# Kernel optimization log

Hardware: AMD Instinct MI355X
Metric: run time of the kernel (lower is better)

Reference implementation:

```python
import jax, jax.numpy as jnp
from jax import lax
import numpy as np

DIM = 384
HEADS = 8
B, H, W = 8, 128, 128
_DN = ('NCHW', 'OIHW', 'NCHW')


def setup_inputs() -> dict:
    key = jax.random.key(0)
    ks = jax.random.split(key, 8)
    x = jax.random.normal(ks[0], (B, DIM, H, W), jnp.float32)
    qkv_w = jax.random.normal(ks[1], (3 * DIM, DIM, 1, 1), jnp.float32) * 0.02
    qkv_b = jax.random.normal(ks[2], (3 * DIM,), jnp.float32) * 0.02
    dw_w = jax.random.normal(ks[3], (3 * DIM, 1, 3, 3), jnp.float32) * 0.02
    dw_b = jax.random.normal(ks[4], (3 * DIM,), jnp.float32) * 0.02
    proj_w = jax.random.normal(ks[5], (DIM, DIM, 1, 1), jnp.float32) * 0.02
    proj_b = jax.random.normal(ks[6], (DIM,), jnp.float32) * 0.02
    temperature = jnp.ones((HEADS, 1, 1), jnp.float32)
    return {"x": x, "qkv_w": qkv_w, "qkv_b": qkv_b, "dw_w": dw_w,
            "dw_b": dw_b, "proj_w": proj_w, "proj_b": proj_b,
            "temperature": temperature}


def _l2norm(t, eps=1e-12):
    # F.normalize(t, dim=-1): divide by max(||t||_2, eps)
    n = jnp.sqrt(jnp.sum(t * t, axis=-1, keepdims=True))
    return t / jnp.maximum(n, eps)


def reference(x, qkv_w, qkv_b, dw_w, dw_b, proj_w, proj_b, temperature):
    b, C, h, w = x.shape
    heads = HEADS
    c = C // heads
    hw = h * w
    # 1x1 pointwise qkv conv
    qkv = lax.conv_general_dilated(x, qkv_w, (1, 1), 'VALID',
                                   dimension_numbers=_DN) + qkv_b[None, :, None, None]
    # 3x3 depthwise conv, padding=1
    qkv = lax.conv_general_dilated(qkv, dw_w, (1, 1), ((1, 1), (1, 1)),
                                   feature_group_count=3 * C,
                                   dimension_numbers=_DN) + dw_b[None, :, None, None]
    q, k, v = jnp.split(qkv, 3, axis=1)
    # b (head c) h w -> b head c (h w)
    q = q.reshape(b, heads, c, hw)
    k = k.reshape(b, heads, c, hw)
    v = v.reshape(b, heads, c, hw)
    q = _l2norm(q)
    k = _l2norm(k)
    # processor scales q by temperature*sqrt(hw); SDPA divides by sqrt(hw):
    # net logits = temperature * q_n @ k_n^T  (CxC channel attention per head)
    temp = temperature.reshape(1, heads, 1, 1)
    logits = jnp.einsum('bhcn,bhdn->bhcd', q * temp, k)
    attn = jax.nn.softmax(logits, axis=-1)
    out = jnp.einsum('bhcd,bhdn->bhcn', attn, v)  # [b, heads, c, hw]
    out = out.reshape(b, C, h, w)
    return lax.conv_general_dilated(out, proj_w, (1, 1), 'VALID',
                                    dimension_numbers=_DN) + proj_b[None, :, None, None]
```

## Files before the change

kernel.cpp:

```cpp
#include <hip/hip_runtime.h>
#include <hip/hip_bf16.h>
#include <cstdint>


#define BATCH 8
#define DIM 384
#define HEADS 8
#define CH 48
#define HW 16384
#define C3 1152

typedef __attribute__((ext_vector_type(8))) short bf16x8;
typedef __attribute__((ext_vector_type(8))) unsigned short u16x8;
typedef __attribute__((ext_vector_type(4))) float f32x4;

__device__ __forceinline__ float b2f(ushort b) {
  union { float f; unsigned u; } x; x.u = ((unsigned)b) << 16; return x.f;
}
__device__ __forceinline__ ushort f2b(float f) {
  union { float f; unsigned u; } x; x.f = f;
  unsigned r = x.u + 0x7fffu + ((x.u >> 16) & 1u);
  return (ushort)(r >> 16);
}

__device__ __forceinline__ void async16(const ushort* g, ushort* l) {
  __builtin_amdgcn_global_load_lds(
      (const __attribute__((address_space(1))) unsigned int*)(unsigned long long)(uintptr_t)g,
      (__attribute__((address_space(3))) unsigned int*)(unsigned int)(uintptr_t)l,
      16, 0, 0);
}

__global__ __launch_bounds__(256) void cast_w(const float* __restrict__ s,
                                              ushort* __restrict__ d, int n) {
  int i = (blockIdx.x * 256 + threadIdx.x) * 4;
  if (i + 3 < n) {
    float4 v = *(const float4*)(s + i);
    ushort4 o = make_ushort4(f2b(v.x), f2b(v.y), f2b(v.z), f2b(v.w));
    *(ushort4*)(d + i) = o;
  }
}

template <typename SrcT, int OUT_BF16>
__global__ __launch_bounds__(512) void gemm_px(
    const ushort* __restrict__ A, const SrcT* __restrict__ src,
    const float* __restrict__ bias, void* __restrict__ Cout,
    int M, long Asb, long Ssb, long Csb) {
  constexpr int K = DIM;
  constexpr int BP = 392;
  int zb = blockIdx.y;
  int px0 = blockIdx.x * 128;
  const ushort* Ab = A + (size_t)zb * Asb;
  const SrcT* Sb = src + (size_t)zb * Ssb;
  __shared__ __align__(16) ushort Bs[128 * BP];
  __shared__ __align__(16) ushort As[2][128 * 64];
  int tid = threadIdx.x, lane = tid & 63, wid = tid >> 6;
  int wm = wid >> 1, wn = wid & 1;
  int fr = lane & 15, fs = lane >> 4;

  {
    int pix = tid & 127;
    int cg = tid >> 7;
#pragma unroll
    for (int rr = 0; rr < 12; ++rr) {
      int c8 = cg + rr * 4;
      u16x8 pk;
#pragma unroll
      for (int j = 0; j < 8; ++j) {
        int c = c8 * 8 + j;
        if constexpr (sizeof(SrcT) == 4)
          pk[j] = f2b(((const float*)Sb)[(size_t)c * HW + px0 + pix]);
        else
          pk[j] = ((const ushort*)Sb)[(size_t)c * HW + px0 + pix];
      }
      *(u16x8*)&Bs[pix * BP + c8 * 8] = pk;
    }
  }

  auto stageA = [&](int buf, int mt, int k0) {
#pragma unroll
    for (int q = 0; q < 2; ++q) {
      int r = q * 64 + wid * 8 + (lane >> 3);
      int col = ((lane & 7) ^ (r & 7)) * 8;
      async16(Ab + (size_t)(mt * 128 + r) * K + k0 + col,
              &As[buf][(q * 64 + wid * 8) * 64]);
    }
  };

  f32x4 acc[2][4];
  auto compute = [&](int buf, int k0) {
#pragma unroll
    for (int kk = 0; kk < 2; ++kk) {
      bf16x8 af[2], bv[4];
#pragma unroll
      for (int m = 0; m < 2; ++m) {
        int R = wm * 32 + m * 16 + fr;
        int slot = kk * 4 + fs;
        af[m] = *(const bf16x8*)&As[buf][R * 64 + ((slot ^ (R & 7)) << 3)];
      }
#pragma unroll
      for (int n = 0; n < 4; ++n) {
        int P = wn * 64 + n * 16 + fr;
        bv[n] = *(const bf16x8*)&Bs[P * BP + k0 + kk * 32 + (fs << 3)];
      }
#pragma unroll
      for (int m = 0; m < 2; ++m)
#pragma unroll
        for (int n = 0; n < 4; ++n)
          acc[m][n] = __builtin_amdgcn_mfma_f32_16x16x32_bf16(af[m], bv[n], acc[m][n], 0, 0, 0);
    }
  };

  const int MT = M >> 7;
  stageA(0, 0, 0);
  __syncthreads();

  for (int mt = 0; mt < MT; ++mt) {
    f32x4 zero = {0.f, 0.f, 0.f, 0.f};
#pragma unroll
    for (int m = 0; m < 2; ++m)
#pragma unroll
      for (int n = 0; n < 4; ++n) acc[m][n] = zero;
#pragma unroll
    for (int t = 0; t < 5; ++t) {
      stageA((t + 1) & 1, mt, (t + 1) * 64);
      __builtin_amdgcn_s_setprio(1);
      compute(t & 1, t * 64);
      __builtin_amdgcn_s_setprio(0);
      __syncthreads();
    }
    if (mt + 1 < MT) stageA(0, mt + 1, 0);
    __builtin_amdgcn_s_setprio(1);
    compute(1, 320);
    __builtin_amdgcn_s_setprio(0);
#pragma unroll
    for (int m = 0; m < 2; ++m)
#pragma unroll
      for (int j = 0; j < 4; ++j) {
        int gr = mt * 128 + wm * 32 + m * 16 + fs * 4 + j;
        float bz = bias[gr];
#pragma unroll
        for (int n = 0; n < 4; ++n) {
          int gc = px0 + wn * 64 + n * 16 + fr;
          float v = acc[m][n][j] + bz;
          if constexpr (OUT_BF16)
            ((ushort*)Cout)[(size_t)zb * Csb + (size_t)gr * HW + gc] = f2b(v);
          else
            ((float*)Cout)[(size_t)zb * Csb + (size_t)gr * HW + gc] = v;
        }
      }
    __syncthreads();
  }
}

__global__ __launch_bounds__(256) void dwconv(
    const ushort* __restrict__ in, const float* __restrict__ w9,
    const float* __restrict__ b9, ushort* __restrict__ out,
    float* __restrict__ sq) {
  int ch = blockIdx.x;
  int b = blockIdx.y;
  const size_t plane = ((size_t)b * C3 + ch) * HW;
  int tid = threadIdx.x, lane = tid & 63;
  int rg = tid >> 4, cg = tid & 15;
  int r0 = rg * 8, c0 = cg * 8;

  float w[9];
#pragma unroll
  for (int i = 0; i < 9; ++i) w[i] = w9[ch * 9 + i];
  float bias = b9[ch];

  float a0[8], a1[8];
#pragma unroll
  for (int c = 0; c < 8; ++c) { a0[c] = 0.f; a1[c] = 0.f; }
  float ss = 0.f;

#pragma unroll
  for (int it = 0; it < 10; ++it) {
    int r = r0 - 1 + it;
    float x[8];
    if ((unsigned)r < 128u) {
      u16x8 raw = *(const u16x8*)(in + plane + (size_t)r * 128 + c0);
#pragma unroll
      for (int c = 0; c < 8; ++c) x[c] = b2f(raw[c]);
    } else {
#pragma unroll
      for (int c = 0; c < 8; ++c) x[c] = 0.f;
    }
    float xl = __shfl(x[7], lane - 1);
    float xr = __shfl(x[0], lane + 1);
    if (cg == 0) xl = 0.f;
    if (cg == 15) xr = 0.f;

    float h0[8], h1[8], h2[8];
#pragma unroll
    for (int c = 0; c < 8; ++c) {
      float l = (c == 0) ? xl : x[c - 1];
      float rt = (c == 7) ? xr : x[c + 1];
      h0[c] = w[0] * l + w[1] * x[c] + w[2] * rt;
      h1[c] = w[3] * l + w[4] * x[c] + w[5] * rt;
      h2[c] = w[6] * l + w[7] * x[c] + w[8] * rt;
    }
    if (it >= 2) {
      int R = r - 1;
      u16x8 pk;
#pragma unroll
      for (int c = 0; c < 8; ++c) {
        float o = a0[c] + h2[c] + bias;
        ss += o * o;
        pk[c] = f2b(o);
      }
      *(u16x8*)(out + plane + (size_t)R * 128 + c0) = pk;
    }
#pragma unroll
    for (int c = 0; c < 8; ++c) { a0[c] = a1[c] + h1[c]; a1[c] = h0[c]; }
  }

  if (ch < 2 * DIM) {
#pragma unroll
    for (int off = 32; off; off >>= 1) ss += __shfl_down(ss, off, 64);
    if (lane == 0) atomicAdd(&sq[b * 2 * DIM + ch], ss);
  }
}

__global__ __launch_bounds__(256) void gram(const ushort* __restrict__ qkvd,
                                            float* __restrict__ G) {
  int chunk = blockIdx.x;
  int bh = blockIdx.y;
  int b = bh >> 3, h = bh & 7;
  int tid = threadIdx.x, lane = tid & 63, wid = tid >> 6;
  const ushort* qbase = qkvd + ((size_t)b * C3 + h * CH) * HW;
  const ushort* kbase = qbase + (size_t)DIM * HW;
  int pix0 = chunk * 1024 + wid * 256;
  int fr = lane & 15, fk = (lane >> 4) * 8;
  f32x4 zero = {0.f, 0.f, 0.f, 0.f};
  f32x4 acc[3][3];
#pragma unroll
  for (int i = 0; i < 3; ++i)
#pragma unroll
    for (int j = 0; j < 3; ++j) acc[i][j] = zero;
#pragma unroll
  for (int it = 0; it < 8; ++it) {
    int pix = pix0 + it * 32 + fk;
    bf16x8 aq[3], bk[3];
#pragma unroll
    for (int mi = 0; mi < 3; ++mi)
      aq[mi] = *(const bf16x8*)(qbase + (size_t)(mi * 16 + fr) * HW + pix);
#pragma unroll
    for (int ni = 0; ni < 3; ++ni)
      bk[ni] = *(const bf16x8*)(kbase + (size_t)(ni * 16 + fr) * HW + pix);
#pragma unroll
    for (int mi = 0; mi < 3; ++mi)
#pragma unroll
      for (int ni = 0; ni < 3; ++ni)
        acc[mi][ni] = __builtin_amdgcn_mfma_f32_16x16x32_bf16(aq[mi], bk[ni], acc[mi][ni], 0, 0, 0);
  }
  __shared__ float gs[CH * CH];
  for (int i = tid; i < CH * CH; i += 256) gs[i] = 0.f;
  __syncthreads();
  int crow = (lane >> 4) * 4, ccol = lane & 15;
#pragma unroll
  for (int mi = 0; mi < 3; ++mi)
#pragma unroll
    for (int ni = 0; ni < 3; ++ni)
#pragma unroll
      for (int j = 0; j < 4; ++j)
        atomicAdd(&gs[(mi * 16 + crow + j) * CH + ni * 16 + ccol], acc[mi][ni][j]);
  __syncthreads();
  float* Gp = G + (size_t)bh * CH * CH;
  for (int i = tid; i < CH * CH; i += 256) atomicAdd(&Gp[i], gs[i]);
}

__global__ void softmax_k(const float* __restrict__ G, const float* __restrict__ sq,
                          const float* __restrict__ temp, float* __restrict__ attn) {
  int bh = blockIdx.x, b = bh >> 3, h = bh & 7;
  int lane = threadIdx.x;
  __shared__ float inq[CH], ink[CH];
  if (lane < CH) {
    inq[lane] = 1.f / fmaxf(sqrtf(sq[b * 2 * DIM + h * CH + lane]), 1e-12f);
    ink[lane] = 1.f / fmaxf(sqrtf(sq[b * 2 * DIM + DIM + h * CH + lane]), 1e-12f);
  }
  __syncthreads();
  if (lane < CH) {
    float t = temp[h] * inq[lane];
    const float* g = G + (size_t)bh * CH * CH + lane * CH;
    float v[CH];
    float mx = -1e30f;
#pragma unroll
    for (int d = 0; d < CH; ++d) { v[d] = t * g[d] * ink[d]; mx = fmaxf(mx, v[d]); }
    float s = 0.f;
#pragma unroll
    for (int d = 0; d < CH; ++d) { v[d] = expf(v[d] - mx); s += v[d]; }
    float inv = 1.f / s;
    float* a = attn + (size_t)bh * CH * CH + lane * CH;
#pragma unroll
    for (int d = 0; d < CH; ++d) a[d] = v[d] * inv;
  }
}

__global__ __launch_bounds__(384) void weff_k(const float* __restrict__ pw,
                                              const float* __restrict__ attn,
                                              ushort* __restrict__ weff) {
  int dg = threadIdx.x;
  int p = blockIdx.x;
  int b = blockIdx.y;
  int h = dg / CH, d = dg - h * CH;
  const float* a = attn + (((size_t)b * HEADS + h) * CH) * CH + d;
  const float* wrow = pw + (size_t)p * DIM + h * CH;
  float s = 0.f;
#pragma unroll
  for (int c = 0; c < CH; ++c) s += wrow[c] * a[c * CH];
  weff[((size_t)b * DIM + p) * DIM + dg] = f2b(s);
}

extern "C" void kernel_launch(void* const* d_in, const int* in_sizes, int n_in,
                              void* d_out, int out_size, void* d_ws, size_t ws_size,
                              hipStream_t stream) {
  const float* x = (const float*)d_in[0];
  const float* qkv_w = (const float*)d_in[1];
  const float* qkv_b = (const float*)d_in[2];
  const float* dw_w = (const float*)d_in[3];
  const float* dw_b = (const float*)d_in[4];
  const float* proj_w = (const float*)d_in[5];
  const float* proj_b = (const float*)d_in[6];
  const float* temp = (const float*)d_in[7];

  const size_t SZ_C1 = (size_t)BATCH * C3 * HW * 2;
  const size_t SZ_WQB = (size_t)C3 * DIM * 2;
  const size_t SZ_SQ = (size_t)BATCH * 2 * DIM * 4;
  const size_t SZ_G = (size_t)BATCH * HEADS * CH * CH * 4;

  const size_t OFF_C1 = 0;
  const size_t OFF_QKVD = OFF_C1 + SZ_C1;
  const size_t OFF_WQB = OFF_QKVD + SZ_C1;
  const size_t OFF_SQ = OFF_WQB + SZ_WQB;
  const size_t OFF_G = OFF_SQ + SZ_SQ;
  const size_t OFF_ATTN = OFF_G + SZ_G;
  const size_t OFF_WEFF = OFF_ATTN + SZ_G;
  const size_t TOTAL = OFF_WEFF + (size_t)BATCH * DIM * DIM * 2;
  if (ws_size < TOTAL) return;

  char* ws = (char*)d_ws;
  ushort* c1 = (ushort*)(ws + OFF_C1);
  ushort* qkvd = (ushort*)(ws + OFF_QKVD);
  ushort* wqb = (ushort*)(ws + OFF_WQB);
  float* sq = (float*)(ws + OFF_SQ);
  float* G = (float*)(ws + OFF_G);
  float* attn = (float*)(ws + OFF_ATTN);
  ushort* weff = (ushort*)(ws + OFF_WEFF);

  hipMemsetAsync(ws + OFF_SQ, 0, SZ_SQ + SZ_G, stream);

  cast_w<<<(C3 * DIM) / 1024, 256, 0, stream>>>(qkv_w, wqb, C3 * DIM);
  gemm_px<float, 1><<<dim3(HW / 128, BATCH), 512, 0, stream>>>(
      wqb, x, qkv_b, (void*)c1, C3, 0L, (long)DIM * HW, (long)C3 * HW);
  dwconv<<<dim3(C3, BATCH), 256, 0, stream>>>(c1, dw_w, dw_b, qkvd, sq);
  gram<<<dim3(16, BATCH * HEADS), 256, 0, stream>>>(qkvd, G);
  softmax_k<<<BATCH * HEADS, 64, 0, stream>>>(G, sq, temp, attn);
  weff_k<<<dim3(DIM, BATCH), 384, 0, stream>>>(proj_w, attn, weff);
  gemm_px<ushort, 0><<<dim3(HW / 128, BATCH), 512, 0, stream>>>(
      weff, qkvd + (size_t)2 * DIM * HW, proj_b, d_out, DIM,
      (long)DIM * DIM, (long)C3 * HW, (long)DIM * HW);
}
```

Before: 543.5 us.

## Enlarge GEMM M-tile to 256 with padded weights and XOR-swizzled B tile

Each block of the pointwise GEMMs now computes 256 output rows per M-step instead of 128, doubling the accumulator tile per wave to raise MFMA work per B-fragment load. The padded B tile (stride 392) is replaced by an unpadded 384-stride layout with an XOR swizzle to avoid LDS bank conflicts while saving shared memory. M is padded (1280 for qkv, 512 for proj) and stores are masked by the real row count, which wastes MFMA work on the padded rows (notably for the proj GEMM, 512 vs 384). The padded weight rows are never written, so they hold uninitialized workspace data, but their outputs are masked off. Shared memory grows and launch bounds force one block per CU.

```diff
diff --git a/kernel.cpp b/kernel.cpp
--- a/kernel.cpp
+++ b/kernel.cpp
@@ -9,6 +9,8 @@
 #define CH 48
 #define HW 16384
 #define C3 1152
+#define MPAD1 1280
+#define WPAD 512
 
 typedef __attribute__((ext_vector_type(8))) short bf16x8;
 typedef __attribute__((ext_vector_type(8))) unsigned short u16x8;
@@ -41,18 +43,17 @@
 }
 
 template <typename SrcT, int OUT_BF16>
-__global__ __launch_bounds__(512) void gemm_px(
+__global__ __launch_bounds__(512, 1) void gemm_px2(
     const ushort* __restrict__ A, const SrcT* __restrict__ src,
     const float* __restrict__ bias, void* __restrict__ Cout,
-    int M, long Asb, long Ssb, long Csb) {
+    int Mpad, int Mreal, long Asb, long Ssb, long Csb) {
   constexpr int K = DIM;
-  constexpr int BP = 392;
   int zb = blockIdx.y;
   int px0 = blockIdx.x * 128;
   const ushort* Ab = A + (size_t)zb * Asb;
   const SrcT* Sb = src + (size_t)zb * Ssb;
-  __shared__ __align__(16) ushort Bs[128 * BP];
-  __shared__ __align__(16) ushort As[2][128 * 64];
+  __shared__ __align__(16) ushort Bs[128 * 384];
+  __shared__ __align__(16) ushort As[2][256 * 64];
   int tid = threadIdx.x, lane = tid & 63, wid = tid >> 6;
   int wm = wid >> 1, wn = wid & 1;
   int fr = lane & 15, fs = lane >> 4;
@@ -72,80 +73,83 @@
         else
           pk[j] = ((const ushort*)Sb)[(size_t)c * HW + px0 + pix];
       }
-      *(u16x8*)&Bs[pix * BP + c8 * 8] = pk;
+      *(u16x8*)&Bs[pix * 384 + ((c8 ^ (pix & 7)) << 3)] = pk;
     }
   }
 
   auto stageA = [&](int buf, int mt, int k0) {
 #pragma unroll
-    for (int q = 0; q < 2; ++q) {
+    for (int q = 0; q < 4; ++q) {
       int r = q * 64 + wid * 8 + (lane >> 3);
       int col = ((lane & 7) ^ (r & 7)) * 8;
-      async16(Ab + (size_t)(mt * 128 + r) * K + k0 + col,
+      async16(Ab + (size_t)(mt * 256 + r) * K + k0 + col,
               &As[buf][(q * 64 + wid * 8) * 64]);
     }
   };
 
-  f32x4 acc[2][4];
-  auto compute = [&](int buf, int k0) {
+  f32x4 acc[4][4];
+  auto compute = [&](int buf, int t) {
 #pragma unroll
     for (int kk = 0; kk < 2; ++kk) {
-      bf16x8 af[2], bv[4];
-#pragma unroll
-      for (int m = 0; m < 2; ++m) {
-        int R = wm * 32 + m * 16 + fr;
+      bf16x8 af[4], bv[4];
+#pragma unroll
+      for (int m = 0; m < 4; ++m) {
+        int R = wm * 64 + m * 16 + fr;
         int slot = kk * 4 + fs;
         af[m] = *(const bf16x8*)&As[buf][R * 64 + ((slot ^ (R & 7)) << 3)];
       }
 #pragma unroll
       for (int n = 0; n < 4; ++n) {
         int P = wn * 64 + n * 16 + fr;
-        bv[n] = *(const bf16x8*)&Bs[P * BP + k0 + kk * 32 + (fs << 3)];
-      }
-#pragma unroll
-      for (int m = 0; m < 2; ++m)
+        int gslot = t * 8 + kk * 4 + fs;
+        bv[n] = *(const bf16x8*)&Bs[P * 384 + ((gslot ^ (P & 7)) << 3)];
+      }
+#pragma unroll
+      for (int m = 0; m < 4; ++m)
 #pragma unroll
         for (int n = 0; n < 4; ++n)
           acc[m][n] = __builtin_amdgcn_mfma_f32_16x16x32_bf16(af[m], bv[n], acc[m][n], 0, 0, 0);
     }
   };
 
-  const int MT = M >> 7;
+  const int MT = Mpad >> 8;
   stageA(0, 0, 0);
   __syncthreads();
 
   for (int mt = 0; mt < MT; ++mt) {
     f32x4 zero = {0.f, 0.f, 0.f, 0.f};
 #pragma unroll
-    for (int m = 0; m < 2; ++m)
+    for (int m = 0; m < 4; ++m)
 #pragma unroll
       for (int n = 0; n < 4; ++n) acc[m][n] = zero;
 #pragma unroll
     for (int t = 0; t < 5; ++t) {
       stageA((t + 1) & 1, mt, (t + 1) * 64);
       __builtin_amdgcn_s_setprio(1);
-      compute(t & 1, t * 64);
+      compute(t & 1, t);
       __builtin_amdgcn_s_setprio(0);
       __syncthreads();
     }
     if (mt + 1 < MT) stageA(0, mt + 1, 0);
     __builtin_amdgcn_s_setprio(1);
-    compute(1, 320);
+    compute(1, 5);
     __builtin_amdgcn_s_setprio(0);
 #pragma unroll
-    for (int m = 0; m < 2; ++m)
+    for (int m = 0; m < 4; ++m)
 #pragma unroll
       for (int j = 0; j < 4; ++j) {
-        int gr = mt * 128 + wm * 32 + m * 16 + fs * 4 + j;
-        float bz = bias[gr];
-#pragma unroll
-        for (int n = 0; n < 4; ++n) {
-          int gc = px0 + wn * 64 + n * 16 + fr;
-          float v = acc[m][n][j] + bz;
-          if constexpr (OUT_BF16)
-            ((ushort*)Cout)[(size_t)zb * Csb + (size_t)gr * HW + gc] = f2b(v);
-          else
-            ((float*)Cout)[(size_t)zb * Csb + (size_t)gr * HW + gc] = v;
+        int gr = mt * 256 + wm * 64 + m * 16 + fs * 4 + j;
+        if (gr < Mreal) {
+          float bz = bias[gr];
+#pragma unroll
+          for (int n = 0; n < 4; ++n) {
+            int gc = px0 + wn * 64 + n * 16 + fr;
+            float v = acc[m][n][j] + bz;
+            if constexpr (OUT_BF16)
+              ((ushort*)Cout)[(size_t)zb * Csb + (size_t)gr * HW + gc] = f2b(v);
+            else
+              ((float*)Cout)[(size_t)zb * Csb + (size_t)gr * HW + gc] = v;
+          }
         }
       }
     __syncthreads();
@@ -308,7 +312,7 @@
   float s = 0.f;
 #pragma unroll
   for (int c = 0; c < CH; ++c) s += wrow[c] * a[c * CH];
-  weff[((size_t)b * DIM + p) * DIM + dg] = f2b(s);
+  weff[((size_t)b * WPAD + p) * DIM + dg] = f2b(s);
 }
 
 extern "C" void kernel_launch(void* const* d_in, const int* in_sizes, int n_in,
@@ -324,9 +328,10 @@
   const float* temp = (const float*)d_in[7];
 
   const size_t SZ_C1 = (size_t)BATCH * C3 * HW * 2;
-  const size_t SZ_WQB = (size_t)C3 * DIM * 2;
+  const size_t SZ_WQB = (size_t)MPAD1 * DIM * 2;
   const size_t SZ_SQ = (size_t)BATCH * 2 * DIM * 4;
   const size_t SZ_G = (size_t)BATCH * HEADS * CH * CH * 4;
+  const size_t SZ_WEFF = (size_t)BATCH * WPAD * DIM * 2;
 
   const size_t OFF_C1 = 0;
   const size_t OFF_QKVD = OFF_C1 + SZ_C1;
@@ -335,7 +340,7 @@
   const size_t OFF_G = OFF_SQ + SZ_SQ;
   const size_t OFF_ATTN = OFF_G + SZ_G;
   const size_t OFF_WEFF = OFF_ATTN + SZ_G;
-  const size_t TOTAL = OFF_WEFF + (size_t)BATCH * DIM * DIM * 2;
+  const size_t TOTAL = OFF_WEFF + SZ_WEFF;
   if (ws_size < TOTAL) return;
 
   char* ws = (char*)d_ws;
@@ -350,13 +355,13 @@
   hipMemsetAsync(ws + OFF_SQ, 0, SZ_SQ + SZ_G, stream);
 
   cast_w<<<(C3 * DIM) / 1024, 256, 0, stream>>>(qkv_w, wqb, C3 * DIM);
-  gemm_px<float, 1><<<dim3(HW / 128, BATCH), 512, 0, stream>>>(
-      wqb, x, qkv_b, (void*)c1, C3, 0L, (long)DIM * HW, (long)C3 * HW);
+  gemm_px2<float, 1><<<dim3(HW / 128, BATCH), 512, 0, stream>>>(
+      wqb, x, qkv_b, (void*)c1, MPAD1, C3, 0L, (long)DIM * HW, (long)C3 * HW);
   dwconv<<<dim3(C3, BATCH), 256, 0, stream>>>(c1, dw_w, dw_b, qkvd, sq);
   gram<<<dim3(16, BATCH * HEADS), 256, 0, stream>>>(qkvd, G);
   softmax_k<<<BATCH * HEADS, 64, 0, stream>>>(G, sq, temp, attn);
   weff_k<<<dim3(DIM, BATCH), 384, 0, stream>>>(proj_w, attn, weff);
-  gemm_px<ushort, 0><<<dim3(HW / 128, BATCH), 512, 0, stream>>>(
-      weff, qkvd + (size_t)2 * DIM * HW, proj_b, d_out, DIM,
-      (long)DIM * DIM, (long)C3 * HW, (long)DIM * HW);
-}
+  gemm_px2<ushort, 0><<<dim3(HW / 128, BATCH), 512, 0, stream>>>(
+      weff, qkvd + (size_t)2 * DIM * HW, proj_b, d_out, WPAD, DIM,
+      (long)WPAD * DIM, (long)C3 * HW, (long)DIM * HW);
+}
```

Measured after the change: 576.1 us. 6.0% more time.
